# Kernel optimization log

Hardware: AMD Instinct MI355X
Metric: run time of the kernel (lower is better)

The kernel has to match this reference:

```python
import jax, jax.numpy as jnp
import numpy as np

EPS = 1e-5

def layernorm(x, w, b):
    mu = x.mean(-1, keepdims=True)
    var = x.var(-1, keepdims=True)
    return (x - mu) / jnp.sqrt(var + EPS) * w + b

def silu(x):
    return x * jax.nn.sigmoid(x)

def causal_dwconv(x, w, b):
    # x: (B,L,D), w: (D,K) depthwise causal conv along L
    K = w.shape[1]
    xt = jnp.moveaxis(x, 1, 2)                      # (B,D,L)
    xt = jnp.pad(xt, ((0, 0), (0, 0), (K - 1, 0)))
    y = jax.lax.conv_general_dilated(xt, w[:, None, :], (1,), 'VALID',
        dimension_numbers=('NCH', 'OIH', 'NCH'), feature_group_count=w.shape[0])
    return jnp.moveaxis(y + b[None, :, None], 2, 1)

def mamba_layer(x, p):
    # LayerNorm + Mamba selective scan; returns (out, C) with C the per-step C projection ("C_fast")
    xn = layernorm(x, p['ln_w'], p['ln_b'])
    xz = xn @ p['in_proj_w']                        # (B,L,2*Di)
    Di = p['conv_w'].shape[0]
    xh, z = xz[..., :Di], xz[..., Di:]
    xh = silu(causal_dwconv(xh, p['conv_w'], p['conv_b']))
    dbl = xh @ p['x_proj_w']                        # (B,L,R+2*S)
    R = p['dt_proj_w'].shape[0]
    S = p['A_log'].shape[1]
    dt = jax.nn.softplus(dbl[..., :R] @ p['dt_proj_w'] + p['dt_proj_b'])  # (B,L,Di)
    Bm = dbl[..., R:R + S]                          # (B,L,S)
    Cm = dbl[..., R + S:]                           # (B,L,S)
    A = -jnp.exp(p['A_log'])                        # (Di,S)
    dA = jnp.exp(dt[..., None] * A)                 # (B,L,Di,S)
    dBx = dt[..., None] * Bm[:, :, None, :] * xh[..., None]
    def step(h, inp):
        a, bx = inp
        h = a * h + bx
        return h, h
    h0 = jnp.zeros((x.shape[0], Di, S), x.dtype)
    _, hs = jax.lax.scan(step, h0, (jnp.moveaxis(dA, 1, 0), jnp.moveaxis(dBx, 1, 0)))
    y = jnp.einsum('lbds,bls->bld', hs, Cm) + p['D'] * xh
    y = y * silu(z)
    return y @ p['out_proj_w'], Cm

def run_chunks(x, k, p):
    # contiguous L-chunks folded into batch (chunks are independent sequences)
    B, L, D = x.shape
    y, C = mamba_layer(x.reshape(B * k, L // k, D), p)
    return y.reshape(B, L, D), C.reshape(B, k, L // k, -1)

def batchnorm(h, g, b):
    mu = h.mean((0, 1))
    var = h.var((0, 1))
    return (h - mu) / jnp.sqrt(var + EPS) * g + b

def freq_ffn(x, fc1_w, bn1_g, bn1_b, r_mat, i_mat, rb, ib, fc2_w, bn2_g, bn2_b):
    h = jax.nn.relu(batchnorm(jnp.einsum('bnc,hc->bnh', x, fc1_w), bn1_g, bn1_b))
    xf = jnp.fft.fft(h, axis=1, norm='ortho')
    # torch einsum 'bnc,cc->bnc' multiplies by the DIAGONAL of the matrix
    rd = jnp.diagonal(r_mat)
    idg = jnp.diagonal(i_mat)
    xr = jax.nn.relu(xf.real * rd - xf.imag * idg + rb)
    xi = jax.nn.relu(xf.imag * rd + xf.real * idg + ib)
    h = jnp.fft.ifft(xr + 1j * xi, axis=1, norm='ortho').real.astype(x.dtype)
    return batchnorm(jnp.einsum('bnh,ch->bnc', h, fc2_w), bn2_g, bn2_b)


def setup_inputs() -> dict:
    key = jax.random.key(0)
    B, L, D = 4, 512, 128
    Di, S, R, K, H = 256, 64, 8, 4, 256
    ks = jax.random.split(key, 16)
    rn = lambda k, sh, s=1.0: (jax.random.normal(k, sh) * s).astype(jnp.float32)
    return {
        'x': rn(ks[0], (B, L, D)),
        'ln_w': jnp.ones((D,), jnp.float32), 'ln_b': jnp.zeros((D,), jnp.float32),
        'in_proj_w': rn(ks[1], (D, 2 * Di), D ** -0.5),
        'conv_w': rn(ks[2], (Di, K), 0.3),
        'conv_b': jnp.zeros((Di,), jnp.float32),
        'x_proj_w': rn(ks[3], (Di, R + 2 * S), Di ** -0.5),
        'dt_proj_w': rn(ks[4], (R, Di), R ** -0.5),
        'dt_proj_b': rn(ks[5], (Di,), 0.1) - 4.0,
        'A_log': jnp.log(jnp.tile(jnp.arange(1, S + 1, dtype=jnp.float32), (Di, 1))),
        'D_param': jnp.ones((Di,), jnp.float32),
        'out_proj_w': rn(ks[6], (Di, D), Di ** -0.5),
        'norm1_w': jnp.ones((D,), jnp.float32), 'norm1_b': jnp.zeros((D,), jnp.float32),
        'norm2_w': jnp.ones((D,), jnp.float32), 'norm2_b': jnp.zeros((D,), jnp.float32),
        'fc1_w': rn(ks[7], (H, D), D ** -0.5),
        'bn1_g': jnp.ones((H,), jnp.float32), 'bn1_b': jnp.zeros((H,), jnp.float32),
        'r_mat': rn(ks[8], (H, H), 0.02),
        'i_mat': rn(ks[9], (H, H), 0.02),
        'rb': rn(ks[10], (H,), 0.02),
        'ib': rn(ks[11], (H,), 0.02),
        'fc2_w': rn(ks[12], (D, H), H ** -0.5),
        'bn2_g': jnp.ones((D,), jnp.float32), 'bn2_b': jnp.zeros((D,), jnp.float32),
    }


def reference(x, ln_w, ln_b, in_proj_w, conv_w, conv_b, x_proj_w, dt_proj_w, dt_proj_b,
              A_log, D_param, out_proj_w, norm1_w, norm1_b, norm2_w, norm2_b,
              fc1_w, bn1_g, bn1_b, r_mat, i_mat, rb, ib, fc2_w, bn2_g, bn2_b):
    p = dict(ln_w=ln_w, ln_b=ln_b, in_proj_w=in_proj_w, conv_w=conv_w, conv_b=conv_b,
             x_proj_w=x_proj_w, dt_proj_w=dt_proj_w, dt_proj_b=dt_proj_b,
             A_log=A_log, D=D_param, out_proj_w=out_proj_w)
    x_o, C0 = mamba_layer(x, p)                 # full sequence
    y1, C1 = run_chunks(x, 2, p)                # 2 halves
    y2, C2 = run_chunks(x, 4, p)                # 4 quarters
    y3, C3 = run_chunks(x, 8, p)                # 8 eighths
    x_o = x_o + y1 + y2 + y3                    # drop_path = Identity
    xo = x + layernorm(x_o, norm1_w, norm1_b)
    out = xo + freq_ffn(layernorm(xo, norm2_w, norm2_b),
                        fc1_w, bn1_g, bn1_b, r_mat, i_mat, rb, ib, fc2_w, bn2_g, bn2_b)
    return out, C0, C1, C2, C3
```

## Files before the change

kernel.cpp:

```cpp
#include <hip/hip_runtime.h>
#include <hip/hip_bf16.h>
#include <math.h>


constexpr int NT = 2048;
constexpr int Di = 256;
constexpr float EPSF = 1e-5f;
constexpr float LOG2E = 1.4426950408889634f;
constexpr float ISQ512 = 0.04419417382415922f;

typedef __attribute__((ext_vector_type(8))) short short8;
typedef __attribute__((ext_vector_type(4))) float f32x4;

constexpr long O_CS2B  = 0;
constexpr long O_CSIB  = 262144;
constexpr long O_A2    = 524288;
constexpr long O_FC1B  = 540672;
constexpr long O_FC2B  = 557056;
constexpr long O_INPB  = 573440;
constexpr long O_XPB   = 606208;
constexpr long O_OPB   = 630784;
constexpr long O_RD    = 647168;
constexpr long O_IDG   = 647424;
constexpr long O_XNB   = 647680;
constexpr long O_XZB   = 778752;
constexpr long O_XHB   = 1827328;
constexpr long O_DBL   = 3924480;
constexpr long O_DTT   = 5038592;
constexpr long O_YS    = 7135744;
constexpr long O_XO    = 9232896;
constexpr long O_LN2B  = 9495040;
constexpr long O_H1    = 9626112;
constexpr long O_H1NTB = 10150400;
constexpr long O_XRI   = 10412544;
constexpr long O_XRITB = 11461120;
constexpr long O_H2B   = 11985408;
constexpr long O_F2    = 12247552;
constexpr long O_SQ1   = 12509696;
constexpr long O_SQ2   = 12510208;
constexpr long O_DXT   = O_H1;
constexpr long O_YACCB = O_F2;
constexpr long O_XO1   = O_H2B;

__device__ __forceinline__ ushort bf16bits(float v) {
  __hip_bfloat16 h = __float2bfloat16(v);
  return *(ushort*)&h;
}
__device__ __forceinline__ float bfu(ushort u) {
  return __uint_as_float((uint)u << 16);
}

__global__ __launch_bounds__(256) void k_tables(
    const float* __restrict__ A_log, const float* __restrict__ fc1_w,
    const float* __restrict__ fc2_w, const float* __restrict__ r_mat,
    const float* __restrict__ i_mat, const float* __restrict__ in_proj_w,
    const float* __restrict__ x_proj_w, const float* __restrict__ out_proj_w,
    const float* __restrict__ x, const float* __restrict__ ln_w,
    const float* __restrict__ ln_b, float* __restrict__ ws) {
  __shared__ float ct[512];
  int tid = threadIdx.x;
  ct[tid]       = cosf((float)tid * (6.283185307179586f / 512.0f)) * ISQ512;
  ct[tid + 256] = cosf((float)(tid + 256) * (6.283185307179586f / 512.0f)) * ISQ512;
  __syncthreads();
  __hip_bfloat16* cs2b = (__hip_bfloat16*)(ws + O_CS2B);
  __hip_bfloat16* csib = (__hip_bfloat16*)(ws + O_CSIB);
  int i = blockIdx.x * 256 + tid;
  if (i < 524288) {
    int r = i >> 9, n = i & 511;
    float v;
    if (r < 512) v = ct[(r * n) & 511];
    else         v = -ct[((r - 512) * n + 384) & 511];
    cs2b[i] = __float2bfloat16(v);
  } else {
    int j = i - 524288;
    int n = j >> 10, kp = j & 1023;
    float v;
    if (kp < 512) v = ct[(n * kp) & 511];
    else          v = -ct[(n * (kp - 512) + 384) & 511];
    csib[j] = __float2bfloat16(v);
  }
  if (i < 16384) ws[O_A2 + i] = -expf(A_log[i]) * LOG2E;
  if (i < 32768) {
    ((__hip_bfloat16*)(ws + O_FC1B))[i] = __float2bfloat16(fc1_w[i]);
    ((__hip_bfloat16*)(ws + O_FC2B))[i] = __float2bfloat16(fc2_w[i]);
  }
  if (i < 65536) {
    int n = i >> 7, k = i & 127;
    ((__hip_bfloat16*)(ws + O_INPB))[i] = __float2bfloat16(in_proj_w[k * 512 + n]);
  }
  if (i < 49152) {
    int n = i >> 8, k = i & 255;
    float v = (n < 136) ? x_proj_w[k * 136 + n] : 0.f;
    ((__hip_bfloat16*)(ws + O_XPB))[i] = __float2bfloat16(v);
  }
  if (i >= 65536 && i < 98304) {
    int j = i - 65536;
    int n = j >> 8, k = j & 255;
    ((__hip_bfloat16*)(ws + O_OPB))[j] = __float2bfloat16(out_proj_w[k * 128 + n]);
  }
  if (i < 256) {
    ws[O_RD + i] = r_mat[i * 256 + i];
    ws[O_IDG + i] = i_mat[i * 256 + i];
  }
  if (i < 512) ws[O_SQ1 + i] = 0.f;
  if (i < 256) ws[O_SQ2 + i] = 0.f;
  if (blockIdx.x < 512) {
    ushort* outb = (ushort*)(ws + O_XNB);
    int lane = tid & 63;
    int t = (blockIdx.x * 256 + tid) >> 6;
    float v0 = x[t * 128 + lane], v1 = x[t * 128 + 64 + lane];
    float s = v0 + v1, sq = v0 * v0 + v1 * v1;
#pragma unroll
    for (int off = 32; off; off >>= 1) { s += __shfl_xor(s, off); sq += __shfl_xor(sq, off); }
    float mu = s * (1.f / 128.f);
    float rstd = rsqrtf(sq * (1.f / 128.f) - mu * mu + EPSF);
    outb[t * 128 + lane]      = bf16bits((v0 - mu) * rstd * ln_w[lane] + ln_b[lane]);
    outb[t * 128 + 64 + lane] = bf16bits((v1 - mu) * rstd * ln_w[64 + lane] + ln_b[64 + lane]);
  }
}

__global__ void k_lndbl(const float* __restrict__ x, const float* __restrict__ xo1,
                        const float* __restrict__ w1, const float* __restrict__ b1,
                        const float* __restrict__ w2, const float* __restrict__ b2,
                        float* __restrict__ xo, ushort* __restrict__ ln2b) {
  int lane = threadIdx.x & 63;
  int t = (blockIdx.x * 256 + threadIdx.x) >> 6;
  float u0 = xo1[t * 128 + lane], u1 = xo1[t * 128 + 64 + lane];
  float s = u0 + u1, sq = u0 * u0 + u1 * u1;
#pragma unroll
  for (int off = 32; off; off >>= 1) { s += __shfl_xor(s, off); sq += __shfl_xor(sq, off); }
  float mu = s * (1.f / 128.f);
  float rstd = rsqrtf(sq * (1.f / 128.f) - mu * mu + EPSF);
  float a0 = x[t * 128 + lane]      + (u0 - mu) * rstd * w1[lane] + b1[lane];
  float a1 = x[t * 128 + 64 + lane] + (u1 - mu) * rstd * w1[64 + lane] + b1[64 + lane];
  xo[t * 128 + lane] = a0;
  xo[t * 128 + 64 + lane] = a1;
  s = a0 + a1; sq = a0 * a0 + a1 * a1;
#pragma unroll
  for (int off = 32; off; off >>= 1) { s += __shfl_xor(s, off); sq += __shfl_xor(sq, off); }
  mu = s * (1.f / 128.f);
  rstd = rsqrtf(sq * (1.f / 128.f) - mu * mu + EPSF);
  ln2b[t * 128 + lane]      = bf16bits((a0 - mu) * rstd * w2[lane] + b2[lane]);
  ln2b[t * 128 + 64 + lane] = bf16bits((a1 - mu) * rstd * w2[64 + lane] + b2[64 + lane]);
}

template <bool OUTBF16>
__global__ __launch_bounds__(256) void k_gmfma(const ushort* __restrict__ A,
                                               const ushort* __restrict__ Bt,
                                               void* __restrict__ Cv,
                                               int M, int N, int K,
                                               long sA, long sBt, long sC) {
  A += (long)blockIdx.z * sA;
  Bt += (long)blockIdx.z * sBt;
  int lane = threadIdx.x & 63, wid = threadIdx.x >> 6;
  int m0 = blockIdx.y * 64 + wid * 16, n0 = blockIdx.x * 64;
  const ushort* arow = A + (long)(m0 + (lane & 15)) * K + (lane >> 4) * 8;
  const ushort* brow = Bt + (long)(n0 + (lane & 15)) * K + (lane >> 4) * 8;
  f32x4 acc0 = {0.f, 0.f, 0.f, 0.f}, acc1 = acc0, acc2 = acc0, acc3 = acc0;
#pragma unroll 4
  for (int k0 = 0; k0 < K; k0 += 32) {
    short8 av = *(const short8*)(arow + k0);
    short8 b0 = *(const short8*)(brow + k0);
    short8 b1 = *(const short8*)(brow + 16L * K + k0);
    short8 b2 = *(const short8*)(brow + 32L * K + k0);
    short8 b3 = *(const short8*)(brow + 48L * K + k0);
    acc0 = __builtin_amdgcn_mfma_f32_16x16x32_bf16(av, b0, acc0, 0, 0, 0);
    acc1 = __builtin_amdgcn_mfma_f32_16x16x32_bf16(av, b1, acc1, 0, 0, 0);
    acc2 = __builtin_amdgcn_mfma_f32_16x16x32_bf16(av, b2, acc2, 0, 0, 0);
    acc3 = __builtin_amdgcn_mfma_f32_16x16x32_bf16(av, b3, acc3, 0, 0, 0);
  }
  int r0 = (lane >> 4) * 4, c0 = lane & 15;
#pragma unroll
  for (int j = 0; j < 4; ++j) {
    long row = m0 + r0 + j;
    float v[4] = {acc0[j], acc1[j], acc2[j], acc3[j]};
    if (OUTBF16) {
      __hip_bfloat16* C = (__hip_bfloat16*)Cv + blockIdx.z * sC;
#pragma unroll
      for (int c = 0; c < 4; ++c) {
        int n = n0 + c * 16 + c0;
        if (n < N) C[row * N + n] = __float2bfloat16(v[c]);
      }
    } else {
      float* C = (float*)Cv + blockIdx.z * sC;
#pragma unroll
      for (int c = 0; c < 4; ++c) {
        int n = n0 + c * 16 + c0;
        if (n < N) C[row * N + n] = v[c];
      }
    }
  }
}

__global__ void k_conv4(const ushort* __restrict__ xzb, const float* __restrict__ cw,
                        const float* __restrict__ cb, ushort* __restrict__ xhb) {
  int i = blockIdx.x * 256 + threadIdx.x;
  int t = i >> 8, d = i & 255;
  float w0 = cw[d * 4 + 0], w1 = cw[d * 4 + 1], w2 = cw[d * 4 + 2], w3 = cw[d * 4 + 3];
  float bias = cb[d];
  float x0  = bfu(xzb[(long)t * 512 + d]);
  float xm1 = t >= 1 ? bfu(xzb[(long)(t - 1) * 512 + d]) : 0.f;
  float xm2 = t >= 2 ? bfu(xzb[(long)(t - 2) * 512 + d]) : 0.f;
  float xm3 = t >= 3 ? bfu(xzb[(long)(t - 3) * 512 + d]) : 0.f;
  if ((t & 63) >= 3) {
    float s = fmaf(w0, xm3, fmaf(w1, xm2, fmaf(w2, xm1, fmaf(w3, x0, bias))));
    float sil = s / (1.f + expf(-s));
    ushort sb = bf16bits(sil);
#pragma unroll
    for (int v = 0; v < 4; ++v) xhb[v * 524288 + i] = sb;
  } else {
#pragma unroll
    for (int v = 0; v < 4; ++v) {
      int lv = t & ((512 >> v) - 1);
      float s = fmaf(w3, x0, bias);
      if (lv >= 1) s = fmaf(w2, xm1, s);
      if (lv >= 2) s = fmaf(w1, xm2, s);
      if (lv >= 3) s = fmaf(w0, xm3, s);
      float sil = s / (1.f + expf(-s));
      xhb[v * 524288 + i] = bf16bits(sil);
    }
  }
}

__global__ __launch_bounds__(256) void k_dtx(const float* __restrict__ dbl,
                                             const ushort* __restrict__ xhb,
                                             const float* __restrict__ w,
                                             const float* __restrict__ bias,
                                             float* __restrict__ DTT,
                                             float* __restrict__ DXT,
                                             float* __restrict__ outC) {
  __shared__ float r8T[8][64];
  __shared__ float xt[64][65];
  __shared__ float wt[8][64];
  int v = blockIdx.z, t0 = blockIdx.y * 64, d0 = blockIdx.x * 64;
  int j = threadIdx.x;
  if (j < 128) {
    int t = j >> 1, half = j & 1;
    float4 q = *(const float4*)&dbl[((long)v * NT + t0 + t) * 136 + half * 4];
    r8T[half * 4 + 0][t] = q.x; r8T[half * 4 + 1][t] = q.y;
    r8T[half * 4 + 2][t] = q.z; r8T[half * 4 + 3][t] = q.w;
  } else {
    int idx = j - 128;
    int r = idx >> 4, dl4 = (idx & 15) * 4;
    float4 q = *(const float4*)&w[r * 256 + d0 + dl4];
    wt[r][dl4] = q.x; wt[r][dl4 + 1] = q.y; wt[r][dl4 + 2] = q.z; wt[r][dl4 + 3] = q.w;
  }
#pragma unroll
  for (int it = 0; it < 4; ++it) {
    int row = (j >> 4) + it * 16, col4 = (j & 15) * 4;
    uint2 u = *(const uint2*)&xhb[((long)v * NT + t0 + row) * 256 + d0 + col4];
    xt[row][col4 + 0] = __uint_as_float(u.x << 16);
    xt[row][col4 + 1] = __uint_as_float(u.x & 0xffff0000u);
    xt[row][col4 + 2] = __uint_as_float(u.y << 16);
    xt[row][col4 + 3] = __uint_as_float(u.y & 0xffff0000u);
  }
  __syncthreads();
  int lane = j & 63, w4 = j >> 6;
#pragma unroll
  for (int k = 0; k < 16; ++k) {
    int dl = w4 * 16 + k, d = d0 + dl;
    float s = bias[d];
#pragma unroll
    for (int r = 0; r < 8; ++r) s = fmaf(r8T[r][lane], wt[r][dl], s);
    float dtv = fmaxf(s, 0.f) + log1pf(expf(-fabsf(s)));
    float dx = dtv * xt[lane][dl];
    long oi = ((long)(v * 256 + d)) * 2048 + t0 + lane;
    DTT[oi] = dtv;
    DXT[oi] = dx;
  }
  if (blockIdx.x == 0) {
#pragma unroll
    for (int k2 = 0; k2 < 16; ++k2) {
      int idx = k2 * 256 + j;
      int tl = idx >> 6, s2 = idx & 63;
      outC[(long)v * 131072 + (long)(t0 + tl) * 64 + s2] =
          dbl[((long)v * NT + t0 + tl) * 136 + 72 + s2];
    }
  }
}

template <int CTRL>
__device__ __forceinline__ float dpp_add(float x) {
  int t = __builtin_amdgcn_update_dpp(0, __float_as_int(x), CTRL, 0xF, 0xF, true);
  return x + __int_as_float(t);
}

__global__ __launch_bounds__(256) void k_scan(const float* __restrict__ DTT,
                                              const float* __restrict__ DXT,
                                              const float* __restrict__ dbl,
                                              const float* __restrict__ A2,
                                              float* __restrict__ ys) {
  int lane = threadIdx.x & 63;
  int gwid = (blockIdx.x * 256 + threadIdx.x) >> 6;
  int v, base;
  if (gwid < 1024)      { v = 0; base = 0; }
  else if (gwid < 3072) { v = 1; base = 1024; }
  else if (gwid < 7168) { v = 2; base = 3072; }
  else                  { v = 3; base = 7168; }
  int local = gwid - base;
  int b = local >> 8, d = local & 255;
  int Lp = 512 >> v;
  int t0 = b * Lp;
  const float* dtrow = DTT + ((long)(v * 256 + d)) * 2048 + t0;
  const float* dxrow = DXT + ((long)(v * 256 + d)) * 2048 + t0;
  const float* dblp = dbl + ((long)v * NT + t0) * 136;
  float* ysp = ys + (long)v * NT * Di + (long)((b << 8) + d) * Lp;
  float a2 = A2[d * 64 + lane];
  float h = 0.f;

#define LOADG(BB, CC, G)                                                     \
  _Pragma("unroll") for (int q = 0; q < 8; ++q) {                            \
    BB[q] = rowp[((G) * 8 + q) * 136 + 8 + lane];                            \
    CC[q] = rowp[((G) * 8 + q) * 136 + 72 + lane];                           \
  }
#define PROCG(BB, CC, G)                                                     \
  _Pragma("unroll") for (int q = 0; q < 8; ++q) {                            \
    int l2 = (G) * 8 + q;                                                    \
    float sdt = __int_as_float(__builtin_amdgcn_readlane(__float_as_int(rdt), l2)); \
    float sdx = __int_as_float(__builtin_amdgcn_readlane(__float_as_int(rdx), l2)); \
    float a = __builtin_amdgcn_exp2f(sdt * a2);                              \
    h = fmaf(a, h, sdx * BB[q]);                                             \
    float p = h * CC[q];                                                     \
    p = dpp_add<0x111>(p); p = dpp_add<0x112>(p);                            \
    p = dpp_add<0x114>(p); p = dpp_add<0x118>(p);                            \
    p = dpp_add<0x142>(p); p = dpp_add<0x143>(p);                            \
    float tot = __int_as_float(__builtin_amdgcn_readlane(__float_as_int(p), 63)); \
    if (lane == l2) ybuf = tot;                                              \
  }

  for (int c = 0; c < Lp; c += 64) {
    float rdt = dtrow[c + lane];
    float rdx = dxrow[c + lane];
    const float* rowp = dblp + (long)c * 136;
    float ybuf = 0.f;
    float b0[8], c0[8], b1[8], c1[8];
    LOADG(b0, c0, 0)
    LOADG(b1, c1, 1)
    PROCG(b0, c0, 0) LOADG(b0, c0, 2)
    PROCG(b1, c1, 1) LOADG(b1, c1, 3)
    PROCG(b0, c0, 2) LOADG(b0, c0, 4)
    PROCG(b1, c1, 3) LOADG(b1, c1, 5)
    PROCG(b0, c0, 4) LOADG(b0, c0, 6)
    PROCG(b1, c1, 5) LOADG(b1, c1, 7)
    PROCG(b0, c0, 6)
    PROCG(b1, c1, 7)
    ysp[c + lane] = ybuf;
  }
#undef LOADG
#undef PROCG
}

__global__ void k_yfull(const float* __restrict__ ys, const ushort* __restrict__ xhb,
                        const ushort* __restrict__ xzb, const float* __restrict__ Dp,
                        ushort* __restrict__ yaccb) {
  int i = blockIdx.x * 256 + threadIdx.x;
  int t = i >> 8, d = i & 255;
  float z = bfu(xzb[(long)t * 512 + 256 + d]);
  float sil = z / (1.f + expf(-z));
  float Dd = Dp[d];
  float s = 0.f;
#pragma unroll
  for (int v = 0; v < 4; ++v) {
    int Lp = 512 >> v;
    int b = t >> (9 - v);
    int l = t & (Lp - 1);
    float ysv = ys[(long)v * NT * Di + (long)((b << 8) + d) * Lp + l];
    float xhv = bfu(xhb[(long)v * 524288 + i]);
    s += ysv + Dd * xhv;
  }
  yaccb[i] = bf16bits(s * sil);
}

template <int F>
__global__ __launch_bounds__(256) void k_bnpart(const float* __restrict__ h,
                                                float* __restrict__ SQ) {
  constexpr int NREP = 256 / F;
  constexpr int TPR = 32 / NREP;
  int tid = threadIdx.x;
  int f = tid & (F - 1), rep = tid / F;
  int t0 = blockIdx.x * 32 + rep * TPR;
  float s = 0.f, q = 0.f;
#pragma unroll
  for (int tt = 0; tt < TPR; ++tt) {
    float v = h[(long)(t0 + tt) * F + f];
    s += v; q += v * v;
  }
  atomicAdd(&SQ[f], s);
  atomicAdd(&SQ[F + f], q);
}

__global__ __launch_bounds__(256) void k_bnreluT(const float* __restrict__ h1,
                                                 const float* __restrict__ SQ,
                                                 const float* __restrict__ g,
                                                 const float* __restrict__ bb,
                                                 ushort* __restrict__ outT) {
  __shared__ float tile[64][65];
  __shared__ float sc_s[64], sh_s[64];
  int t0 = blockIdx.x * 64, f0 = blockIdx.y * 64, b = blockIdx.z;
  int tid = threadIdx.x;
  if (tid < 64) {
    int f = f0 + tid;
    float mu = SQ[f] * (1.f / NT);
    float var = SQ[256 + f] * (1.f / NT) - mu * mu;
    float sc = g[f] * rsqrtf(var + EPSF);
    sc_s[tid] = sc;
    sh_s[tid] = bb[f] - mu * sc;
  }
  __syncthreads();
#pragma unroll
  for (int i = 0; i < 16; ++i) {
    int idx = i * 256 + tid;
    int r = idx >> 6, c = idx & 63;
    float v = h1[((long)(b * 512 + t0 + r)) * 256 + f0 + c];
    tile[r][c] = fmaxf(fmaf(v, sc_s[c], sh_s[c]), 0.f);
  }
  __syncthreads();
  int tc2 = (tid & 31) * 2, fr0 = tid >> 5;
#pragma unroll
  for (int i = 0; i < 8; ++i) {
    int fr = fr0 + i * 8;
    uint u = ((uint)bf16bits(tile[tc2 + 1][fr]) << 16) | bf16bits(tile[tc2][fr]);
    long off = (long)b * 131072 + (long)(f0 + fr) * 512 + t0 + tc2;
    *(uint*)(outT + off) = u;
  }
}

__global__ __launch_bounds__(256) void k_freqT(const float* __restrict__ XRI,
                                               const float* __restrict__ rd,
                                               const float* __restrict__ idg,
                                               const float* __restrict__ rb,
                                               const float* __restrict__ ib,
                                               ushort* __restrict__ outT) {
  __shared__ float tr[64][65], ti[64][65];
  int n0 = blockIdx.x * 64, f0 = blockIdx.y * 64, b = blockIdx.z;
  int tid = threadIdx.x;
#pragma unroll
  for (int i = 0; i < 16; ++i) {
    int idx = i * 256 + tid;
    int r = idx >> 6, c = idx & 63;
    int f = f0 + c;
    long base = (long)b * 262144 + (long)(n0 + r) * 256 + f;
    float a = XRI[base], b2 = XRI[base + 131072];
    tr[r][c] = fmaxf(a * rd[f] - b2 * idg[f] + rb[f], 0.f);
    ti[r][c] = fmaxf(b2 * rd[f] + a * idg[f] + ib[f], 0.f);
  }
  __syncthreads();
  int tc2 = (tid & 31) * 2, fr0 = tid >> 5;
#pragma unroll
  for (int i = 0; i < 8; ++i) {
    int fr = fr0 + i * 8;
    long offr = (long)b * 262144 + (long)(f0 + fr) * 1024 + n0 + tc2;
    uint ur = ((uint)bf16bits(tr[tc2 + 1][fr]) << 16) | bf16bits(tr[tc2][fr]);
    uint ui = ((uint)bf16bits(ti[tc2 + 1][fr]) << 16) | bf16bits(ti[tc2][fr]);
    *(uint*)(outT + offr) = ur;
    *(uint*)(outT + offr + 512) = ui;
  }
}

__global__ __launch_bounds__(256) void k_final(const float* __restrict__ xo,
                                               const float* __restrict__ f2,
                                               const float* __restrict__ SQ,
                                               const float* __restrict__ g,
                                               const float* __restrict__ bb,
                                               float* __restrict__ out) {
  __shared__ float sc_s[128], sh_s[128];
  int tid = threadIdx.x;
  if (tid < 128) {
    float mu = SQ[tid] * (1.f / NT);
    float var = SQ[128 + tid] * (1.f / NT) - mu * mu;
    float sc = g[tid] * rsqrtf(var + EPSF);
    sc_s[tid] = sc;
    sh_s[tid] = bb[tid] - mu * sc;
  }
  __syncthreads();
  int i = blockIdx.x * 256 + tid;
  int c = i & 127;
  out[i] = xo[i] + fmaf(f2[i], sc_s[c], sh_s[c]);
}

extern "C" void kernel_launch(void* const* d_in, const int* in_sizes, int n_in,
                              void* d_out, int out_size, void* d_ws, size_t ws_size,
                              hipStream_t stream) {
  const float* x         = (const float*)d_in[0];
  const float* ln_w      = (const float*)d_in[1];
  const float* ln_b      = (const float*)d_in[2];
  const float* in_proj_w = (const float*)d_in[3];
  const float* conv_w    = (const float*)d_in[4];
  const float* conv_b    = (const float*)d_in[5];
  const float* x_proj_w  = (const float*)d_in[6];
  const float* dt_proj_w = (const float*)d_in[7];
  const float* dt_proj_b = (const float*)d_in[8];
  const float* A_log     = (const float*)d_in[9];
  const float* D_param   = (const float*)d_in[10];
  const float* out_proj_w= (const float*)d_in[11];
  const float* n1w       = (const float*)d_in[12];
  const float* n1b       = (const float*)d_in[13];
  const float* n2w       = (const float*)d_in[14];
  const float* n2b       = (const float*)d_in[15];
  const float* fc1_w     = (const float*)d_in[16];
  const float* bn1_g     = (const float*)d_in[17];
  const float* bn1_b     = (const float*)d_in[18];
  const float* r_mat     = (const float*)d_in[19];
  const float* i_mat     = (const float*)d_in[20];
  const float* rb        = (const float*)d_in[21];
  const float* ib        = (const float*)d_in[22];
  const float* fc2_w     = (const float*)d_in[23];
  const float* bn2_g     = (const float*)d_in[24];
  const float* bn2_b     = (const float*)d_in[25];
  float* ws  = (float*)d_ws;
  float* out = (float*)d_out;

  k_tables<<<4096, 256, 0, stream>>>(A_log, fc1_w, fc2_w, r_mat, i_mat,
                                     in_proj_w, x_proj_w, out_proj_w,
                                     x, ln_w, ln_b, ws);
  k_gmfma<true><<<dim3(8, 32, 1), 256, 0, stream>>>(
      (const ushort*)(ws + O_XNB), (const ushort*)(ws + O_INPB), ws + O_XZB,
      2048, 512, 128, 0, 0, 0);
  k_conv4<<<2048, 256, 0, stream>>>((const ushort*)(ws + O_XZB), conv_w, conv_b,
                                    (ushort*)(ws + O_XHB));
  k_gmfma<false><<<dim3(3, 32, 4), 256, 0, stream>>>(
      (const ushort*)(ws + O_XHB), (const ushort*)(ws + O_XPB), ws + O_DBL,
      2048, 136, 256, 524288L, 0, 278528L);
  k_dtx<<<dim3(4, 32, 4), 256, 0, stream>>>(ws + O_DBL, (const ushort*)(ws + O_XHB),
                                            dt_proj_w, dt_proj_b, ws + O_DTT,
                                            ws + O_DXT, out + 262144);
  k_scan<<<3840, 256, 0, stream>>>(ws + O_DTT, ws + O_DXT, ws + O_DBL,
                                   ws + O_A2, ws + O_YS);
  k_yfull<<<2048, 256, 0, stream>>>(ws + O_YS, (const ushort*)(ws + O_XHB),
                                    (const ushort*)(ws + O_XZB), D_param,
                                    (ushort*)(ws + O_YACCB));
  k_gmfma<false><<<dim3(2, 32, 1), 256, 0, stream>>>(
      (const ushort*)(ws + O_YACCB), (const ushort*)(ws + O_OPB), ws + O_XO1,
      2048, 128, 256, 0, 0, 0);
  k_lndbl<<<512, 256, 0, stream>>>(x, ws + O_XO1, n1w, n1b, n2w, n2b,
                                   ws + O_XO, (ushort*)(ws + O_LN2B));
  k_gmfma<false><<<dim3(4, 32, 1), 256, 0, stream>>>(
      (const ushort*)(ws + O_LN2B), (const ushort*)(ws + O_FC1B), ws + O_H1,
      2048, 256, 128, 0, 0, 0);
  k_bnpart<256><<<64, 256, 0, stream>>>(ws + O_H1, ws + O_SQ1);
  k_bnreluT<<<dim3(8, 4, 4), 256, 0, stream>>>(ws + O_H1, ws + O_SQ1, bn1_g,
                                               bn1_b, (ushort*)(ws + O_H1NTB));
  k_gmfma<false><<<dim3(4, 16, 4), 256, 0, stream>>>(
      (const ushort*)(ws + O_CS2B), (const ushort*)(ws + O_H1NTB), ws + O_XRI,
      1024, 256, 512, 0, 131072L, 262144L);
  k_freqT<<<dim3(8, 4, 4), 256, 0, stream>>>(ws + O_XRI, ws + O_RD, ws + O_IDG,
                                             rb, ib, (ushort*)(ws + O_XRITB));
  k_gmfma<true><<<dim3(4, 8, 4), 256, 0, stream>>>(
      (const ushort*)(ws + O_CSIB), (const ushort*)(ws + O_XRITB), ws + O_H2B,
      512, 256, 1024, 0, 262144L, 131072L);
  k_gmfma<false><<<dim3(2, 32, 1), 256, 0, stream>>>(
      (const ushort*)(ws + O_H2B), (const ushort*)(ws + O_FC2B), ws + O_F2,
      2048, 128, 256, 0, 0, 0);
  k_bnpart<128><<<64, 256, 0, stream>>>(ws + O_F2, ws + O_SQ2);
  k_final<<<1024, 256, 0, stream>>>(ws + O_XO, ws + O_F2, ws + O_SQ2,
                                    bn2_g, bn2_b, out);
}
```

Measured before the change: 292.7 us.

## Fold dt_proj into x_proj GEMM, pack dt/dx, fuse BN stats and DFT epilogue

Precomputes the product x_proj·dt_proj so the dt logits come straight out of an enlarged x_proj GEMM. A new prep kernel packs dt and dt*x as bf16 pairs and builds a contiguous B/C buffer for the scan, which now reads one word per step instead of two. Batchnorm statistics are accumulated with atomics in a new GEMM epilogue that writes bf16, removing the separate bnpart passes. The forward DFT GEMM is fused with the frequency mixing and transpose. Storing several intermediates in bf16 and merging the weight matrices change rounding and may cost some accuracy.

```diff
diff --git a/kernel.cpp b/kernel.cpp
--- a/kernel.cpp
+++ b/kernel.cpp
@@ -18,29 +18,28 @@
 constexpr long O_FC1B  = 540672;
 constexpr long O_FC2B  = 557056;
 constexpr long O_INPB  = 573440;
-constexpr long O_XPB   = 606208;
-constexpr long O_OPB   = 630784;
-constexpr long O_RD    = 647168;
-constexpr long O_IDG   = 647424;
-constexpr long O_XNB   = 647680;
-constexpr long O_XZB   = 778752;
-constexpr long O_XHB   = 1827328;
-constexpr long O_DBL   = 3924480;
-constexpr long O_DTT   = 5038592;
-constexpr long O_YS    = 7135744;
-constexpr long O_XO    = 9232896;
-constexpr long O_LN2B  = 9495040;
-constexpr long O_H1    = 9626112;
-constexpr long O_H1NTB = 10150400;
-constexpr long O_XRI   = 10412544;
-constexpr long O_XRITB = 11461120;
-constexpr long O_H2B   = 11985408;
-constexpr long O_F2    = 12247552;
-constexpr long O_SQ1   = 12509696;
-constexpr long O_SQ2   = 12510208;
-constexpr long O_DXT   = O_H1;
-constexpr long O_YACCB = O_F2;
-constexpr long O_XO1   = O_H2B;
+constexpr long O_XPB2  = 606208;
+constexpr long O_OPB   = 663552;
+constexpr long O_RD    = 679936;
+constexpr long O_IDG   = 680192;
+constexpr long O_XNB   = 680448;
+constexpr long O_XZB   = 811520;
+constexpr long O_XHB   = 1335808;
+constexpr long O_DBLX  = 2384384;
+constexpr long O_DTDX  = 5595648;
+constexpr long O_BCT   = 7692800;
+constexpr long O_YS    = 8741376;
+constexpr long O_XO    = 10838528;
+constexpr long O_LN2B  = 11100672;
+constexpr long O_H1B   = 11231744;
+constexpr long O_H1NTB = 11493888;
+constexpr long O_XRITB = 11756032;
+constexpr long O_H2B   = 12280320;
+constexpr long O_F2B   = 12542464;
+constexpr long O_SQ1   = 12673536;
+constexpr long O_SQ2   = 12674048;
+constexpr long O_XO1   = O_XRITB;
+constexpr long O_YACCB = O_DBLX;
 
 __device__ __forceinline__ ushort bf16bits(float v) {
   __hip_bfloat16 h = __float2bfloat16(v);
@@ -54,13 +53,14 @@
     const float* __restrict__ A_log, const float* __restrict__ fc1_w,
     const float* __restrict__ fc2_w, const float* __restrict__ r_mat,
     const float* __restrict__ i_mat, const float* __restrict__ in_proj_w,
-    const float* __restrict__ x_proj_w, const float* __restrict__ out_proj_w,
+    const float* __restrict__ x_proj_w, const float* __restrict__ dt_proj_w,
+    const float* __restrict__ out_proj_w,
     const float* __restrict__ x, const float* __restrict__ ln_w,
     const float* __restrict__ ln_b, float* __restrict__ ws) {
   __shared__ float ct[512];
   int tid = threadIdx.x;
-  ct[tid]       = cosf((float)tid * (6.283185307179586f / 512.0f)) * ISQ512;
-  ct[tid + 256] = cosf((float)(tid + 256) * (6.283185307179586f / 512.0f)) * ISQ512;
+  ct[tid]       = __cosf((float)tid * (6.283185307179586f / 512.0f)) * ISQ512;
+  ct[tid + 256] = __cosf((float)(tid + 256) * (6.283185307179586f / 512.0f)) * ISQ512;
   __syncthreads();
   __hip_bfloat16* cs2b = (__hip_bfloat16*)(ws + O_CS2B);
   __hip_bfloat16* csib = (__hip_bfloat16*)(ws + O_CSIB);
@@ -88,13 +88,19 @@
     int n = i >> 7, k = i & 127;
     ((__hip_bfloat16*)(ws + O_INPB))[i] = __float2bfloat16(in_proj_w[k * 512 + n]);
   }
-  if (i < 49152) {
+  if (i < 114688) {
     int n = i >> 8, k = i & 255;
-    float v = (n < 136) ? x_proj_w[k * 136 + n] : 0.f;
-    ((__hip_bfloat16*)(ws + O_XPB))[i] = __float2bfloat16(v);
-  }
-  if (i >= 65536 && i < 98304) {
-    int j = i - 65536;
+    float v = 0.f;
+    if (n < 136) v = x_proj_w[k * 136 + n];
+    else if (n < 392) {
+      int d = n - 136;
+#pragma unroll
+      for (int r = 0; r < 8; ++r) v = fmaf(x_proj_w[k * 136 + r], dt_proj_w[r * 256 + d], v);
+    }
+    ((__hip_bfloat16*)(ws + O_XPB2))[i] = __float2bfloat16(v);
+  }
+  if (i >= 131072 && i < 163840) {
+    int j = i - 131072;
     int n = j >> 8, k = j & 255;
     ((__hip_bfloat16*)(ws + O_OPB))[j] = __float2bfloat16(out_proj_w[k * 128 + n]);
   }
@@ -192,6 +198,49 @@
   }
 }
 
+__global__ __launch_bounds__(256) void k_gmfma_bn(const ushort* __restrict__ A,
+                                                  const ushort* __restrict__ Bt,
+                                                  ushort* __restrict__ C,
+                                                  float* __restrict__ SQ,
+                                                  int N, int K) {
+  int lane = threadIdx.x & 63, wid = threadIdx.x >> 6;
+  int m0 = blockIdx.y * 64 + wid * 16, n0 = blockIdx.x * 64;
+  const ushort* arow = A + (long)(m0 + (lane & 15)) * K + (lane >> 4) * 8;
+  const ushort* brow = Bt + (long)(n0 + (lane & 15)) * K + (lane >> 4) * 8;
+  f32x4 acc[4] = {{0.f, 0.f, 0.f, 0.f}, {0.f, 0.f, 0.f, 0.f},
+                  {0.f, 0.f, 0.f, 0.f}, {0.f, 0.f, 0.f, 0.f}};
+#pragma unroll 4
+  for (int k0 = 0; k0 < K; k0 += 32) {
+    short8 av = *(const short8*)(arow + k0);
+#pragma unroll
+    for (int c = 0; c < 4; ++c) {
+      short8 bv = *(const short8*)(brow + (long)c * 16 * K + k0);
+      acc[c] = __builtin_amdgcn_mfma_f32_16x16x32_bf16(av, bv, acc[c], 0, 0, 0);
+    }
+  }
+  int r0 = (lane >> 4) * 4, c0 = lane & 15;
+#pragma unroll
+  for (int j = 0; j < 4; ++j) {
+    long row = m0 + r0 + j;
+#pragma unroll
+    for (int c = 0; c < 4; ++c)
+      C[row * N + n0 + c * 16 + c0] = bf16bits(acc[c][j]);
+  }
+#pragma unroll
+  for (int c = 0; c < 4; ++c) {
+    f32x4 v = acc[c];
+    float s = v[0] + v[1] + v[2] + v[3];
+    float q = v[0] * v[0] + v[1] * v[1] + v[2] * v[2] + v[3] * v[3];
+    s += __shfl_xor(s, 16); s += __shfl_xor(s, 32);
+    q += __shfl_xor(q, 16); q += __shfl_xor(q, 32);
+    if ((lane >> 4) == 0) {
+      int n = n0 + c * 16 + c0;
+      atomicAdd(&SQ[n], s);
+      atomicAdd(&SQ[N + n], q);
+    }
+  }
+}
+
 __global__ void k_conv4(const ushort* __restrict__ xzb, const float* __restrict__ cw,
                         const float* __restrict__ cb, ushort* __restrict__ xhb) {
   int i = blockIdx.x * 256 + threadIdx.x;
@@ -222,60 +271,50 @@
   }
 }
 
-__global__ __launch_bounds__(256) void k_dtx(const float* __restrict__ dbl,
-                                             const ushort* __restrict__ xhb,
-                                             const float* __restrict__ w,
-                                             const float* __restrict__ bias,
-                                             float* __restrict__ DTT,
-                                             float* __restrict__ DXT,
-                                             float* __restrict__ outC) {
-  __shared__ float r8T[8][64];
-  __shared__ float xt[64][65];
-  __shared__ float wt[8][64];
-  int v = blockIdx.z, t0 = blockIdx.y * 64, d0 = blockIdx.x * 64;
-  int j = threadIdx.x;
-  if (j < 128) {
-    int t = j >> 1, half = j & 1;
-    float4 q = *(const float4*)&dbl[((long)v * NT + t0 + t) * 136 + half * 4];
-    r8T[half * 4 + 0][t] = q.x; r8T[half * 4 + 1][t] = q.y;
-    r8T[half * 4 + 2][t] = q.z; r8T[half * 4 + 3][t] = q.w;
-  } else {
-    int idx = j - 128;
-    int r = idx >> 4, dl4 = (idx & 15) * 4;
-    float4 q = *(const float4*)&w[r * 256 + d0 + dl4];
-    wt[r][dl4] = q.x; wt[r][dl4 + 1] = q.y; wt[r][dl4 + 2] = q.z; wt[r][dl4 + 3] = q.w;
-  }
-#pragma unroll
-  for (int it = 0; it < 4; ++it) {
-    int row = (j >> 4) + it * 16, col4 = (j & 15) * 4;
-    uint2 u = *(const uint2*)&xhb[((long)v * NT + t0 + row) * 256 + d0 + col4];
-    xt[row][col4 + 0] = __uint_as_float(u.x << 16);
-    xt[row][col4 + 1] = __uint_as_float(u.x & 0xffff0000u);
-    xt[row][col4 + 2] = __uint_as_float(u.y << 16);
-    xt[row][col4 + 3] = __uint_as_float(u.y & 0xffff0000u);
-  }
-  __syncthreads();
-  int lane = j & 63, w4 = j >> 6;
-#pragma unroll
-  for (int k = 0; k < 16; ++k) {
-    int dl = w4 * 16 + k, d = d0 + dl;
-    float s = bias[d];
-#pragma unroll
-    for (int r = 0; r < 8; ++r) s = fmaf(r8T[r][lane], wt[r][dl], s);
-    float dtv = fmaxf(s, 0.f) + log1pf(expf(-fabsf(s)));
-    float dx = dtv * xt[lane][dl];
-    long oi = ((long)(v * 256 + d)) * 2048 + t0 + lane;
-    DTT[oi] = dtv;
-    DXT[oi] = dx;
-  }
-  if (blockIdx.x == 0) {
-#pragma unroll
-    for (int k2 = 0; k2 < 16; ++k2) {
-      int idx = k2 * 256 + j;
-      int tl = idx >> 6, s2 = idx & 63;
-      outC[(long)v * 131072 + (long)(t0 + tl) * 64 + s2] =
-          dbl[((long)v * NT + t0 + tl) * 136 + 72 + s2];
-    }
+__global__ __launch_bounds__(256) void k_prep(const float* __restrict__ dblx,
+                                              const ushort* __restrict__ xhb,
+                                              const float* __restrict__ dt_b,
+                                              float* __restrict__ outC,
+                                              uint* __restrict__ DTDX,
+                                              float* __restrict__ BCT) {
+  int v = blockIdx.y, t0 = blockIdx.x * 64;
+  int tid = threadIdx.x;
+  const float* dp = dblx + ((long)v * 2048 + t0) * 392;
+  float* bout = BCT + ((long)v * 2048 + t0) * 128;
+#pragma unroll
+  for (int it = 0; it < 32; ++it) {
+    int idx = it * 256 + tid;
+    int t = idx >> 7, j = idx & 127;
+    bout[idx] = dp[(long)t * 392 + 8 + j];
+  }
+#pragma unroll
+  for (int it = 0; it < 16; ++it) {
+    int idx = it * 256 + tid;
+    int t = idx >> 6, s = idx & 63;
+    outC[(long)v * 131072 + (long)(t0 + t) * 64 + s] = dp[(long)t * 392 + 72 + s];
+  }
+  __shared__ uint tile[64][65];
+#pragma unroll
+  for (int dc = 0; dc < 4; ++dc) {
+    int d0 = dc * 64;
+#pragma unroll
+    for (int it = 0; it < 16; ++it) {
+      int idx = it * 256 + tid;
+      int t = idx >> 6, dl = idx & 63;
+      int d = d0 + dl;
+      float logit = dp[(long)t * 392 + 136 + d] + dt_b[d];
+      float dtv = fmaxf(logit, 0.f) + log1pf(expf(-fabsf(logit)));
+      float xv = bfu(xhb[((long)v * 2048 + t0 + t) * 256 + d]);
+      tile[t][dl] = ((uint)bf16bits(dtv * xv) << 16) | (uint)bf16bits(dtv);
+    }
+    __syncthreads();
+#pragma unroll
+    for (int it = 0; it < 16; ++it) {
+      int idx = it * 256 + tid;
+      int dl = idx >> 6, t = idx & 63;
+      DTDX[((long)(v * 256 + d0 + dl)) * 2048 + t0 + t] = tile[t][dl];
+    }
+    __syncthreads();
   }
 }
 
@@ -285,9 +324,8 @@
   return x + __int_as_float(t);
 }
 
-__global__ __launch_bounds__(256) void k_scan(const float* __restrict__ DTT,
-                                              const float* __restrict__ DXT,
-                                              const float* __restrict__ dbl,
+__global__ __launch_bounds__(256) void k_scan(const uint* __restrict__ DTDX,
+                                              const float* __restrict__ BCT,
                                               const float* __restrict__ A2,
                                               float* __restrict__ ys) {
   int lane = threadIdx.x & 63;
@@ -301,38 +339,38 @@
   int b = local >> 8, d = local & 255;
   int Lp = 512 >> v;
   int t0 = b * Lp;
-  const float* dtrow = DTT + ((long)(v * 256 + d)) * 2048 + t0;
-  const float* dxrow = DXT + ((long)(v * 256 + d)) * 2048 + t0;
-  const float* dblp = dbl + ((long)v * NT + t0) * 136;
+  const uint* drow = DTDX + ((long)(v * 256 + d)) * 2048 + t0;
+  const float* brow = BCT + ((long)(v * 2048 + t0)) * 128;
   float* ysp = ys + (long)v * NT * Di + (long)((b << 8) + d) * Lp;
   float a2 = A2[d * 64 + lane];
   float h = 0.f;
 
 #define LOADG(BB, CC, G)                                                     \
-  _Pragma("unroll") for (int q = 0; q < 8; ++q) {                            \
-    BB[q] = rowp[((G) * 8 + q) * 136 + 8 + lane];                            \
-    CC[q] = rowp[((G) * 8 + q) * 136 + 72 + lane];                           \
-  }
+  { const float* rg = rowp + (G) * 1024;                                     \
+    _Pragma("unroll") for (int q = 0; q < 8; ++q) {                          \
+      BB[q] = rg[q * 128 + lane];                                            \
+      CC[q] = rg[q * 128 + 64 + lane];                                       \
+    } }
 #define PROCG(BB, CC, G)                                                     \
   _Pragma("unroll") for (int q = 0; q < 8; ++q) {                            \
-    int l2 = (G) * 8 + q;                                                    \
-    float sdt = __int_as_float(__builtin_amdgcn_readlane(__float_as_int(rdt), l2)); \
-    float sdx = __int_as_float(__builtin_amdgcn_readlane(__float_as_int(rdx), l2)); \
+    const int l2 = (G) * 8 + q;                                              \
+    uint u = (uint)__builtin_amdgcn_readlane((int)rdx, l2);                  \
+    float sdt = __uint_as_float(u << 16);                                    \
+    float sdx = __uint_as_float(u & 0xffff0000u);                            \
     float a = __builtin_amdgcn_exp2f(sdt * a2);                              \
     h = fmaf(a, h, sdx * BB[q]);                                             \
     float p = h * CC[q];                                                     \
     p = dpp_add<0x111>(p); p = dpp_add<0x112>(p);                            \
     p = dpp_add<0x114>(p); p = dpp_add<0x118>(p);                            \
     p = dpp_add<0x142>(p); p = dpp_add<0x143>(p);                            \
-    float tot = __int_as_float(__builtin_amdgcn_readlane(__float_as_int(p), 63)); \
-    if (lane == l2) ybuf = tot;                                              \
+    int tot = __builtin_amdgcn_readlane(__float_as_int(p), 63);              \
+    asm("v_writelane_b32 %0, %1, %2" : "+v"(ybuf_i) : "s"(tot), "i"(l2));    \
   }
 
   for (int c = 0; c < Lp; c += 64) {
-    float rdt = dtrow[c + lane];
-    float rdx = dxrow[c + lane];
-    const float* rowp = dblp + (long)c * 136;
-    float ybuf = 0.f;
+    uint rdx = drow[c + lane];
+    const float* rowp = brow + (long)c * 128;
+    int ybuf_i = 0;
     float b0[8], c0[8], b1[8], c1[8];
     LOADG(b0, c0, 0)
     LOADG(b1, c1, 1)
@@ -344,7 +382,7 @@
     PROCG(b1, c1, 5) LOADG(b1, c1, 7)
     PROCG(b0, c0, 6)
     PROCG(b1, c1, 7)
-    ysp[c + lane] = ybuf;
+    ysp[c + lane] = __int_as_float(ybuf_i);
   }
 #undef LOADG
 #undef PROCG
@@ -371,25 +409,7 @@
   yaccb[i] = bf16bits(s * sil);
 }
 
-template <int F>
-__global__ __launch_bounds__(256) void k_bnpart(const float* __restrict__ h,
-                                                float* __restrict__ SQ) {
-  constexpr int NREP = 256 / F;
-  constexpr int TPR = 32 / NREP;
-  int tid = threadIdx.x;
-  int f = tid & (F - 1), rep = tid / F;
-  int t0 = blockIdx.x * 32 + rep * TPR;
-  float s = 0.f, q = 0.f;
-#pragma unroll
-  for (int tt = 0; tt < TPR; ++tt) {
-    float v = h[(long)(t0 + tt) * F + f];
-    s += v; q += v * v;
-  }
-  atomicAdd(&SQ[f], s);
-  atomicAdd(&SQ[F + f], q);
-}
-
-__global__ __launch_bounds__(256) void k_bnreluT(const float* __restrict__ h1,
+__global__ __launch_bounds__(256) void k_bnreluT(const ushort* __restrict__ h1b,
                                                  const float* __restrict__ SQ,
                                                  const float* __restrict__ g,
                                                  const float* __restrict__ bb,
@@ -407,12 +427,15 @@
     sh_s[tid] = bb[f] - mu * sc;
   }
   __syncthreads();
-#pragma unroll
-  for (int i = 0; i < 16; ++i) {
+  const uint* h1u = (const uint*)h1b;
+#pragma unroll
+  for (int i = 0; i < 8; ++i) {
     int idx = i * 256 + tid;
-    int r = idx >> 6, c = idx & 63;
-    float v = h1[((long)(b * 512 + t0 + r)) * 256 + f0 + c];
-    tile[r][c] = fmaxf(fmaf(v, sc_s[c], sh_s[c]), 0.f);
+    int r = idx >> 5, cu = idx & 31;
+    uint u = h1u[((long)(b * 512 + t0 + r)) * 128 + (f0 >> 1) + cu];
+    int c = cu * 2;
+    tile[r][c]     = fmaxf(fmaf(bfu((ushort)(u & 0xffff)), sc_s[c], sh_s[c]), 0.f);
+    tile[r][c + 1] = fmaxf(fmaf(bfu((ushort)(u >> 16)), sc_s[c + 1], sh_s[c + 1]), 0.f);
   }
   __syncthreads();
   int tc2 = (tid & 31) * 2, fr0 = tid >> 5;
@@ -425,40 +448,57 @@
   }
 }
 
-__global__ __launch_bounds__(256) void k_freqT(const float* __restrict__ XRI,
-                                               const float* __restrict__ rd,
-                                               const float* __restrict__ idg,
-                                               const float* __restrict__ rb,
-                                               const float* __restrict__ ib,
-                                               ushort* __restrict__ outT) {
-  __shared__ float tr[64][65], ti[64][65];
-  int n0 = blockIdx.x * 64, f0 = blockIdx.y * 64, b = blockIdx.z;
-  int tid = threadIdx.x;
-#pragma unroll
-  for (int i = 0; i < 16; ++i) {
-    int idx = i * 256 + tid;
-    int r = idx >> 6, c = idx & 63;
-    int f = f0 + c;
-    long base = (long)b * 262144 + (long)(n0 + r) * 256 + f;
-    float a = XRI[base], b2 = XRI[base + 131072];
-    tr[r][c] = fmaxf(a * rd[f] - b2 * idg[f] + rb[f], 0.f);
-    ti[r][c] = fmaxf(b2 * rd[f] + a * idg[f] + ib[f], 0.f);
-  }
-  __syncthreads();
-  int tc2 = (tid & 31) * 2, fr0 = tid >> 5;
-#pragma unroll
-  for (int i = 0; i < 8; ++i) {
-    int fr = fr0 + i * 8;
-    long offr = (long)b * 262144 + (long)(f0 + fr) * 1024 + n0 + tc2;
-    uint ur = ((uint)bf16bits(tr[tc2 + 1][fr]) << 16) | bf16bits(tr[tc2][fr]);
-    uint ui = ((uint)bf16bits(ti[tc2 + 1][fr]) << 16) | bf16bits(ti[tc2][fr]);
-    *(uint*)(outT + offr) = ur;
-    *(uint*)(outT + offr + 512) = ui;
+__global__ __launch_bounds__(256) void k_dftfreq(const ushort* __restrict__ CS2B,
+                                                 const ushort* __restrict__ H1NTB,
+                                                 const float* __restrict__ rd,
+                                                 const float* __restrict__ idg,
+                                                 const float* __restrict__ rb,
+                                                 const float* __restrict__ ib,
+                                                 ushort* __restrict__ XRITB) {
+  int b = blockIdx.z;
+  int lane = threadIdx.x & 63, wid = threadIdx.x >> 6;
+  int m0 = blockIdx.y * 64 + wid * 16;
+  int n0 = blockIdx.x * 64;
+  const ushort* acrow = CS2B + (long)(m0 + (lane & 15)) * 512 + (lane >> 4) * 8;
+  const ushort* asrow = acrow + 512L * 512;
+  const ushort* brow = H1NTB + (long)b * 131072 + (long)(n0 + (lane & 15)) * 512 + (lane >> 4) * 8;
+  f32x4 aC[4] = {{0.f, 0.f, 0.f, 0.f}, {0.f, 0.f, 0.f, 0.f},
+                 {0.f, 0.f, 0.f, 0.f}, {0.f, 0.f, 0.f, 0.f}};
+  f32x4 aS[4] = {{0.f, 0.f, 0.f, 0.f}, {0.f, 0.f, 0.f, 0.f},
+                 {0.f, 0.f, 0.f, 0.f}, {0.f, 0.f, 0.f, 0.f}};
+#pragma unroll 2
+  for (int k0 = 0; k0 < 512; k0 += 32) {
+    short8 avc = *(const short8*)(acrow + k0);
+    short8 avs = *(const short8*)(asrow + k0);
+#pragma unroll
+    for (int c = 0; c < 4; ++c) {
+      short8 bv = *(const short8*)(brow + (long)c * 16 * 512 + k0);
+      aC[c] = __builtin_amdgcn_mfma_f32_16x16x32_bf16(avc, bv, aC[c], 0, 0, 0);
+      aS[c] = __builtin_amdgcn_mfma_f32_16x16x32_bf16(avs, bv, aS[c], 0, 0, 0);
+    }
+  }
+  int r0 = (lane >> 4) * 4, c0 = lane & 15;
+#pragma unroll
+  for (int c = 0; c < 4; ++c) {
+    int f = n0 + c * 16 + c0;
+    float rdv = rd[f], idv = idg[f], rbv = rb[f], ibv = ib[f];
+    ushort pr[4], pi[4];
+#pragma unroll
+    for (int j = 0; j < 4; ++j) {
+      float xr = aC[c][j], xi = aS[c][j];
+      pr[j] = bf16bits(fmaxf(xr * rdv - xi * idv + rbv, 0.f));
+      pi[j] = bf16bits(fmaxf(xi * rdv + xr * idv + ibv, 0.f));
+    }
+    long base = (long)b * 262144 + (long)f * 1024 + m0 + r0;
+    uint2 ur = make_uint2(((uint)pr[1] << 16) | pr[0], ((uint)pr[3] << 16) | pr[2]);
+    uint2 ui = make_uint2(((uint)pi[1] << 16) | pi[0], ((uint)pi[3] << 16) | pi[2]);
+    *(uint2*)(XRITB + base) = ur;
+    *(uint2*)(XRITB + base + 512) = ui;
   }
 }
 
 __global__ __launch_bounds__(256) void k_final(const float* __restrict__ xo,
-                                               const float* __restrict__ f2,
+                                               const ushort* __restrict__ f2b,
                                                const float* __restrict__ SQ,
                                                const float* __restrict__ g,
                                                const float* __restrict__ bb,
@@ -475,7 +515,7 @@
   __syncthreads();
   int i = blockIdx.x * 256 + tid;
   int c = i & 127;
-  out[i] = xo[i] + fmaf(f2[i], sc_s[c], sh_s[c]);
+  out[i] = xo[i] + fmaf(bfu(f2b[i]), sc_s[c], sh_s[c]);
 }
 
 extern "C" void kernel_launch(void* const* d_in, const int* in_sizes, int n_in,
@@ -511,20 +551,20 @@
   float* out = (float*)d_out;
 
   k_tables<<<4096, 256, 0, stream>>>(A_log, fc1_w, fc2_w, r_mat, i_mat,
-                                     in_proj_w, x_proj_w, out_proj_w,
+                                     in_proj_w, x_proj_w, dt_proj_w, out_proj_w,
                                      x, ln_w, ln_b, ws);
   k_gmfma<true><<<dim3(8, 32, 1), 256, 0, stream>>>(
       (const ushort*)(ws + O_XNB), (const ushort*)(ws + O_INPB), ws + O_XZB,
       2048, 512, 128, 0, 0, 0);
   k_conv4<<<2048, 256, 0, stream>>>((const ushort*)(ws + O_XZB), conv_w, conv_b,
                                     (ushort*)(ws + O_XHB));
-  k_gmfma<false><<<dim3(3, 32, 4), 256, 0, stream>>>(
-      (const ushort*)(ws + O_XHB), (const ushort*)(ws + O_XPB), ws + O_DBL,
-      2048, 136, 256, 524288L, 0, 278528L);
-  k_dtx<<<dim3(4, 32, 4), 256, 0, stream>>>(ws + O_DBL, (const ushort*)(ws + O_XHB),
-                                            dt_proj_w, dt_proj_b, ws + O_DTT,
-                                            ws + O_DXT, out + 262144);
-  k_scan<<<3840, 256, 0, stream>>>(ws + O_DTT, ws + O_DXT, ws + O_DBL,
+  k_gmfma<false><<<dim3(7, 32, 4), 256, 0, stream>>>(
+      (const ushort*)(ws + O_XHB), (const ushort*)(ws + O_XPB2), ws + O_DBLX,
+      2048, 392, 256, 524288L, 0, 802816L);
+  k_prep<<<dim3(32, 4), 256, 0, stream>>>(ws + O_DBLX, (const ushort*)(ws + O_XHB),
+                                          dt_proj_b, out + 262144,
+                                          (uint*)(ws + O_DTDX), ws + O_BCT);
+  k_scan<<<3840, 256, 0, stream>>>((const uint*)(ws + O_DTDX), ws + O_BCT,
                                    ws + O_A2, ws + O_YS);
   k_yfull<<<2048, 256, 0, stream>>>(ws + O_YS, (const ushort*)(ws + O_XHB),
                                     (const ushort*)(ws + O_XZB), D_param,
@@ -534,24 +574,21 @@
       2048, 128, 256, 0, 0, 0);
   k_lndbl<<<512, 256, 0, stream>>>(x, ws + O_XO1, n1w, n1b, n2w, n2b,
                                    ws + O_XO, (ushort*)(ws + O_LN2B));
-  k_gmfma<false><<<dim3(4, 32, 1), 256, 0, stream>>>(
-      (const ushort*)(ws + O_LN2B), (const ushort*)(ws + O_FC1B), ws + O_H1,
-      2048, 256, 128, 0, 0, 0);
-  k_bnpart<256><<<64, 256, 0, stream>>>(ws + O_H1, ws + O_SQ1);
-  k_bnreluT<<<dim3(8, 4, 4), 256, 0, stream>>>(ws + O_H1, ws + O_SQ1, bn1_g,
-                                               bn1_b, (ushort*)(ws + O_H1NTB));
-  k_gmfma<false><<<dim3(4, 16, 4), 256, 0, stream>>>(
-      (const ushort*)(ws + O_CS2B), (const ushort*)(ws + O_H1NTB), ws + O_XRI,
-      1024, 256, 512, 0, 131072L, 262144L);
-  k_freqT<<<dim3(8, 4, 4), 256, 0, stream>>>(ws + O_XRI, ws + O_RD, ws + O_IDG,
-                                             rb, ib, (ushort*)(ws + O_XRITB));
+  k_gmfma_bn<<<dim3(4, 32), 256, 0, stream>>>(
+      (const ushort*)(ws + O_LN2B), (const ushort*)(ws + O_FC1B),
+      (ushort*)(ws + O_H1B), ws + O_SQ1, 256, 128);
+  k_bnreluT<<<dim3(8, 4, 4), 256, 0, stream>>>((const ushort*)(ws + O_H1B),
+                                               ws + O_SQ1, bn1_g, bn1_b,
+                                               (ushort*)(ws + O_H1NTB));
+  k_dftfreq<<<dim3(4, 8, 4), 256, 0, stream>>>(
+      (const ushort*)(ws + O_CS2B), (const ushort*)(ws + O_H1NTB),
+      ws + O_RD, ws + O_IDG, rb, ib, (ushort*)(ws + O_XRITB));
   k_gmfma<true><<<dim3(4, 8, 4), 256, 0, stream>>>(
       (const ushort*)(ws + O_CSIB), (const ushort*)(ws + O_XRITB), ws + O_H2B,
       512, 256, 1024, 0, 262144L, 131072L);
-  k_gmfma<false><<<dim3(2, 32, 1), 256, 0, stream>>>(
-      (const ushort*)(ws + O_H2B), (const ushort*)(ws + O_FC2B), ws + O_F2,
-      2048, 128, 256, 0, 0, 0);
-  k_bnpart<128><<<64, 256, 0, stream>>>(ws + O_F2, ws + O_SQ2);
-  k_final<<<1024, 256, 0, stream>>>(ws + O_XO, ws + O_F2, ws + O_SQ2,
-                                    bn2_g, bn2_b, out);
-}
+  k_gmfma_bn<<<dim3(2, 32), 256, 0, stream>>>(
+      (const ushort*)(ws + O_H2B), (const ushort*)(ws + O_FC2B),
+      (ushort*)(ws + O_F2B), ws + O_SQ2, 128, 256);
+  k_final<<<1024, 256, 0, stream>>>(ws + O_XO, (const ushort*)(ws + O_F2B),
+                                    ws + O_SQ2, bn2_g, bn2_b, out);
+}
```

Result: slower. 347.8 us (+18.8%).
